# Performance work log

Hardware: AMD Instinct MI355X
Metric: run time of the kernel (lower is better)

The kernel has to match this reference:

```python
import jax, jax.numpy as jnp
import numpy as np
import math

S = 72; IMG_W = 640; IMG_H = 360; STRIDE = 16
IN_CH = 256; AFC = 64
FMAP_H = IMG_H // STRIDE  # 22
FMAP_W = IMG_W // STRIDE  # 40
N_OFFSETS = S
LEFT_ANGLES = [72., 60., 49., 39., 30., 22.]
RIGHT_ANGLES = [108., 120., 131., 141., 150., 158.]
BOTTOM_ANGLES = [165., 150., 141., 131., 120., 108., 100., 90., 80., 72., 60., 49., 39., 30., 15.]
BATCH = 8


def _gen_anchor(start, angle, cut):
    n = FMAP_H if cut else N_OFFSETS
    ys = np.linspace(1., 0., n)
    a = np.zeros(5 + n)
    sx, sy = start
    a[2] = 1. - sy
    a[3] = sx
    a[5:] = (sx + (1. - ys - 1. + sy) / math.tan(angle * math.pi / 180.)) * IMG_W
    return a


def _gen_side(angles, nb, x=None, y=None):
    if x is None:
        starts = [(xx, y) for xx in np.linspace(1., 0., nb)]
    else:
        starts = [(x, yy) for yy in np.linspace(1., 0., nb)]
    anc = np.stack([_gen_anchor(s, a, False) for s in starts for a in angles])
    cut = np.stack([_gen_anchor(s, a, True) for s in starts for a in angles])
    return anc, cut


def build_anchor_tables():
    la, lc = _gen_side(LEFT_ANGLES, 72, x=0.)
    ra, rc = _gen_side(RIGHT_ANGLES, 72, x=1.)
    ba, bc = _gen_side(BOTTOM_ANGLES, 128, y=1.)
    anchors = np.concatenate([la, ba, ra]).astype(np.float32)  # [P, 5+S]
    cuts = np.concatenate([lc, bc, rc])                        # [P, 5+fmap_h]
    xs = np.flip(np.round(cuts[:, 5:] / STRIDE), axis=1).astype(np.int64)
    cut_xs = np.clip(xs, 0, FMAP_W - 1).astype(np.int32)       # [P, fmap_h]
    invalid = (xs < 0) | (xs > FMAP_W)                         # faithful to original (> not >=)
    return anchors, cut_xs, invalid


def setup_inputs():
    key = jax.random.key(0)
    ks = jax.random.split(key, 6)
    anchors, cut_xs, invalid = build_anchor_tables()
    P = anchors.shape[0]  # 2784
    D = AFC * FMAP_H      # 1408
    s = 0.02
    return {
        "x": jax.random.normal(ks[0], (BATCH, IN_CH, FMAP_H, FMAP_W), jnp.float32),
        "conv_w": jax.random.normal(ks[1], (AFC, IN_CH), jnp.float32) * s,
        "conv_b": jnp.zeros((AFC,), jnp.float32),
        "att_w": jax.random.normal(ks[2], (P - 1, D), jnp.float32) * s,
        "att_b": jnp.zeros((P - 1,), jnp.float32),
        "cls_w": jax.random.normal(ks[3], (2, 2 * D), jnp.float32) * s,
        "cls_b": jnp.zeros((2,), jnp.float32),
        "so_w": jax.random.normal(ks[4], (1, 2 * D), jnp.float32) * s,
        "so_b": jnp.zeros((1,), jnp.float32),
        "reg_w": jax.random.normal(ks[5], (N_OFFSETS + 1, 2 * D), jnp.float32) * s,
        "reg_b": jnp.zeros((N_OFFSETS + 1,), jnp.float32),
        "anchors": jnp.asarray(anchors),
        "cut_xs": jnp.asarray(cut_xs),
        "invalid_mask": jnp.asarray(invalid),
    }


def reference(x, conv_w, conv_b, att_w, att_b, cls_w, cls_b, so_w, so_b, reg_w, reg_b, anchors, cut_xs, invalid_mask):
    B = x.shape[0]
    P, H = cut_xs.shape
    # 1x1 conv
    feat = jnp.einsum('bchw,oc->bohw', x, conv_w) + conv_b[None, :, None, None]
    # fused anchor feature gather: rois[b,p,c,h] = feat[b,c,h,cut_xs[p,h]]
    rois = feat[:, :, jnp.arange(H)[None, :], cut_xs]           # [B,C,P,H]
    rois = jnp.transpose(rois, (0, 2, 1, 3))                    # [B,P,C,H]
    rois = jnp.where(invalid_mask[None, :, None, :], 0., rois)
    D = rois.shape[2] * H
    baf = rois.reshape(B, P, D)
    scores = baf.reshape(B * P, D) @ att_w.T + att_b
    attention = jax.nn.softmax(scores, axis=1).reshape(B, P, P - 1)
    # off-diagonal scatter (replaces torch eye/nonzero trick): M[b,i,j]=attention[b,i,j'] for j!=i, diag 0
    i_idx = jnp.arange(P)[:, None]
    j_off = jnp.arange(P - 1)[None, :]
    tgt_j = jnp.where(j_off < i_idx, j_off, j_off + 1)          # [P,P-1]
    M = jnp.zeros((B, P, P), x.dtype).at[:, jnp.broadcast_to(i_idx, (P, P - 1)), tgt_j].set(attention)
    # (baf^T @ M^T)^T == M @ baf
    att_feats = jnp.einsum('bpq,bqd->bpd', M, baf)
    feats = jnp.concatenate([att_feats, baf], axis=2).reshape(B * P, 2 * D)
    cls = (feats @ cls_w.T + cls_b).reshape(B, P, 2)
    so = jax.nn.sigmoid(feats @ so_w.T + so_b).reshape(B, P, 1)
    reg = (feats @ reg_w.T + reg_b).reshape(B, P, N_OFFSETS + 1)
    anc = jnp.broadcast_to(anchors[None], (B, P, anchors.shape[1]))
    reg_proposals = jnp.concatenate([cls, (anc[:, :, 2:3] + so) * 0.5, anc[:, :, 3:4], anc[:, :, 4:] + reg], axis=2)
    return reg_proposals, M, feat
```

## Files before the change

### kernel.cpp

```cpp
#include <hip/hip_runtime.h>
#include <stdint.h>

#define PTOT 2784
#define PM1  2783
#define DDIM 1408
#define NB   8
#define ROWS 22272
#define KHEAD 2816
#define MROW 2816
#define BTROWS 1536

typedef __attribute__((ext_vector_type(8))) short bf16x8;
typedef __attribute__((ext_vector_type(4))) float f32x4;
typedef long i64f8;

__device__ __forceinline__ short f2bf_rne(float x) {
    uint32_t u = __float_as_uint(x);
    u += 0x7fffu + ((u >> 16) & 1u);
    return (short)(u >> 16);
}
__device__ __forceinline__ float bf2f(short s) {
    return __uint_as_float((uint32_t)(unsigned short)s << 16);
}

__device__ __forceinline__ unsigned char f2e4m3(float x) {
    uint32_t u = __float_as_uint(x);
    uint32_t sgn = (u >> 24) & 0x80u;
    uint32_t ax = u & 0x7fffffffu;
    ax += 0x7ffffu + ((ax >> 20) & 1u);
    if (ax >= 0x43E80000u) return (unsigned char)(sgn | 0x7Eu);
    if (ax < 0x3C800000u) return (unsigned char)sgn;
    uint32_t e = (ax >> 23) - 120u;
    uint32_t m = (ax >> 20) & 7u;
    return (unsigned char)(sgn | (e << 3) | m);
}

__device__ __forceinline__ void gld16(const void* g, void* l) {
    __builtin_amdgcn_global_load_lds(
        (const __attribute__((address_space(1))) void*)(uintptr_t)g,
        (__attribute__((address_space(3))) void*)(uint32_t)(uintptr_t)l,
        16, 0, 0);
}

#define VMW(N) asm volatile("s_waitcnt vmcnt(" #N ")" ::: "memory")

__global__ __launch_bounds__(256) void k_conv(
    const float* __restrict__ x, const float* __restrict__ w,
    const float* __restrict__ cb, float* __restrict__ feat) {
  __shared__ float xs[256 * 32];
  int b = blockIdx.x / 28;
  int t0 = (blockIdx.x % 28) * 32;
  int t = threadIdx.x;
  for (int i = t; i < 256 * 32; i += 256) {
    int c = i >> 5, pos = i & 31;
    int hw = t0 + pos;
    xs[i] = (hw < 880) ? x[((size_t)b * 256 + c) * 880 + hw] : 0.f;
  }
  __syncthreads();
  int o = t & 63, g = t >> 6;
  float acc[8];
#pragma unroll
  for (int pp = 0; pp < 8; ++pp) acc[pp] = cb[o];
  const float* wr = w + o * 256;
  for (int c = 0; c < 256; ++c) {
    float wv = wr[c];
#pragma unroll
    for (int pp = 0; pp < 8; ++pp) acc[pp] += wv * xs[c * 32 + g + pp * 4];
  }
#pragma unroll
  for (int pp = 0; pp < 8; ++pp) {
    int hw = t0 + g + pp * 4;
    if (hw < 880) feat[((size_t)b * 64 + o) * 880 + hw] = acc[pp];
  }
}

__global__ __launch_bounds__(256) void k_prep(
    const float* __restrict__ att_w, const float* __restrict__ cls_w,
    const float* __restrict__ so_w, const float* __restrict__ reg_w,
    const float* __restrict__ cls_b, const float* __restrict__ so_b,
    const float* __restrict__ reg_b,
    short* __restrict__ attw, short* __restrict__ wbf,
    float* __restrict__ bias80, float* __restrict__ M,
    unsigned char* __restrict__ Mbf8, unsigned char* __restrict__ bafT8,
    short* __restrict__ Msc) {
  const int64_t n_attw = (int64_t)2816 * DDIM;
  const int64_t n_w = 80 * (int64_t)KHEAD;
  const int64_t n_pa = (int64_t)NB * MROW * 32;
  const int64_t n_pb = (int64_t)NB * BTROWS * 32;
  const int64_t total = n_attw + n_w + 80 + ROWS + n_pa + n_pb;
  for (int64_t i = (int64_t)blockIdx.x * 256 + threadIdx.x; i < total;
       i += (int64_t)gridDim.x * 256) {
    if (i < n_attw) {
      int j = (int)(i / DDIM), k = (int)(i - (int64_t)j * DDIM);
      float v = (j < PM1) ? att_w[(size_t)j * DDIM + k] : 0.f;
      attw[i] = f2bf_rne(v);
    } else if (i < n_attw + n_w) {
      int64_t ii = i - n_attw;
      int n = (int)(ii / KHEAD), k = (int)(ii - (int64_t)n * KHEAD);
      float v = 0.f;
      if (n < 2) v = cls_w[n * KHEAD + k];
      else if (n == 2) v = so_w[k];
      else if (n < 76) v = reg_w[(size_t)(n - 3) * KHEAD + k];
      wbf[ii] = f2bf_rne(v);
    } else if (i < n_attw + n_w + 80) {
      int n = (int)(i - n_attw - n_w);
      float v = 0.f;
      if (n < 2) v = cls_b[n];
      else if (n == 2) v = so_b[0];
      else if (n < 76) v = reg_b[n - 3];
      bias80[n] = v;
    } else if (i < n_attw + n_w + 80 + ROWS) {
      int r = (int)(i - n_attw - n_w - 80);
      int p = r % PTOT;
      M[(size_t)r * PTOT + p] = -1e30f;
      if (Msc) Msc[(size_t)r * PTOT + p] = f2bf_rne(-1e30f);
    } else if (i < n_attw + n_w + 80 + ROWS + n_pa) {
      int64_t ii = i - n_attw - n_w - 80 - ROWS;
      int64_t row = ii >> 5; int c = (int)(ii & 31);
      Mbf8[row * 2816 + 2784 + c] = 0;
    } else {
      int64_t ii = i - n_attw - n_w - 80 - ROWS - n_pa;
      int64_t row = ii >> 5; int c = (int)(ii & 31);
      bafT8[row * 2816 + 2784 + c] = 0;
    }
  }
}

__global__ __launch_bounds__(256) void k_gather(
    const float* __restrict__ feat, const int* __restrict__ cutx,
    const unsigned char* __restrict__ inval,
    short* __restrict__ baf, unsigned char* __restrict__ bafT8) {
  int p0 = blockIdx.x * 64, d0 = blockIdx.y * 64, b = blockIdx.z;
  __shared__ short tile[64][72];
  int t = threadIdx.x;
  for (int i = t; i < 64 * 64; i += 256) {
    int pl = i >> 6, dl = i & 63;
    int p = p0 + pl, d = d0 + dl;
    float v = 0.f;
    if (p < PTOT && d < DDIM) {
      int c = d / 22, h = d - c * 22;
      if (!inval[p * 22 + h]) {
        int xc = cutx[p * 22 + h];
        v = feat[(((size_t)b * 64 + c) * 22 + h) * 40 + xc];
      }
    }
    tile[pl][dl] = f2bf_rne(v);
  }
  __syncthreads();
  if (d0 < DDIM) {
    for (int u = t; u < 512; u += 256) {
      int pl = u >> 3, dg = u & 7;
      int p = p0 + pl;
      if (p < PTOT) {
        bf16x8 v;
#pragma unroll
        for (int e = 0; e < 8; ++e) v[e] = tile[pl][dg * 8 + e];
        *(bf16x8*)&baf[((size_t)b * PTOT + p) * DDIM + d0 + dg * 8] = v;
      }
    }
  }
  for (int u = t; u < 512; u += 256) {
    int dl = u >> 3, pg = u & 7;
    int pbase = p0 + pg * 8;
    if (pbase + 7 < PTOT) {
      unsigned long long pk = 0;
#pragma unroll
      for (int e = 0; e < 8; ++e) {
        float fv = bf2f(tile[pg * 8 + e][dl]);
        pk |= (unsigned long long)f2e4m3(fv) << (8 * e);
      }
      *(unsigned long long*)&bafT8[((size_t)b * BTROWS + d0 + dl) * 2816 + pbase] = pk;
    }
  }
}

#define SC_TILE(OFF_, S_, SN_, STAGE_, VM_)                                    \
  {                                                                            \
    const char* cb_ = sm + (S_) * 16384;                                       \
    if (STAGE_) {                                                              \
      char* nb_ = sm + (SN_) * 16384;                                          \
      gld16(gA0 + (OFF_), nb_ + dd0);                                          \
      gld16(gA1 + (OFF_), nb_ + dd1);                                          \
      gld16(gB0 + (OFF_), nb_ + 8192 + dd0);                                   \
      gld16(gB1 + (OFF_), nb_ + 8192 + dd1);                                   \
    }                                                                          \
    if ((VM_) == 8) VMW(8); else if ((VM_) == 4) VMW(4); else VMW(0);          \
    __builtin_amdgcn_s_barrier();                                              \
    bf16x8 av[4], bv[4];                                                       \
    _Pragma("unroll") for (int i = 0; i < 4; ++i)                              \
      av[i] = *(const bf16x8*)(cb_ + offA[i]);                                 \
    _Pragma("unroll") for (int i = 0; i < 4; ++i)                              \
      bv[i] = *(const bf16x8*)(cb_ + 8192 + offB[i]);                          \
    _Pragma("unroll") for (int mi = 0; mi < 4; ++mi)                           \
      _Pragma("unroll") for (int ni = 0; ni < 4; ++ni)                         \
        acc[mi][ni] = __builtin_amdgcn_mfma_f32_16x16x32_bf16(                 \
            av[mi], bv[ni], acc[mi][ni], 0, 0, 0);                             \
    __builtin_amdgcn_s_barrier();                                              \
  }

template<int OUTMODE>
__global__ __launch_bounds__(256) void k_scores(
    const short* __restrict__ baf, const short* __restrict__ attw,
    const float* __restrict__ att_b, float* __restrict__ Mout,
    short* __restrict__ Msc) {
  __shared__ char sm[49152];
  int wg = blockIdx.x;
  int xcd = wg & 7, lin = wg >> 3;
  int wgid = (xcd < 4) ? xcd * 479 + lin : 1916 + (xcd - 4) * 478 + lin;
  int it = wgid / 22, nt = wgid - it * 22;
  int m0 = it * 128, n0 = nt * 128;

  int t = threadIdx.x, w = t >> 6, l = t & 63;
  int lr = l & 15, lg = l >> 4;
  int wr = w >> 1, wc = w & 1;

  const char* gA0; const char* gA1; const char* gB0; const char* gB1;
  int dd0, dd1;
  {
    int o0 = w * 2048 + l * 16;
    int o1 = o0 + 1024;
    int r0_ = o0 >> 6, c0 = (o0 & 63) ^ (((o0 >> 7) & 3) << 4);
    int r1_ = o1 >> 6, c1 = (o1 & 63) ^ (((o1 >> 7) & 3) << 4);
    gA0 = (const char*)(baf + (size_t)(m0 + r0_) * DDIM) + c0;
    gA1 = (const char*)(baf + (size_t)(m0 + r1_) * DDIM) + c1;
    gB0 = (const char*)(attw + (size_t)(n0 + r0_) * DDIM) + c0;
    gB1 = (const char*)(attw + (size_t)(n0 + r1_) * DDIM) + c1;
    dd0 = o0; dd1 = o1;
  }
  int offA[4], offB[4];
#pragma unroll
  for (int i = 0; i < 4; ++i) {
    int xa = (wr * 64 + i * 16 + lr) * 64 + lg * 16;
    offA[i] = xa ^ (((xa >> 7) & 3) << 4);
    int xb = (wc * 64 + i * 16 + lr) * 64 + lg * 16;
    offB[i] = xb ^ (((xb >> 7) & 3) << 4);
  }

  f32x4 acc[4][4];
  const f32x4 fz = {0.f, 0.f, 0.f, 0.f};
#pragma unroll
  for (int mi = 0; mi < 4; ++mi)
#pragma unroll
    for (int ni = 0; ni < 4; ++ni) acc[mi][ni] = fz;

  gld16(gA0, sm + dd0);            gld16(gA1, sm + dd1);
  gld16(gB0, sm + 8192 + dd0);     gld16(gB1, sm + 8192 + dd1);
  gld16(gA0 + 64, sm + 16384 + dd0);        gld16(gA1 + 64, sm + 16384 + dd1);
  gld16(gB0 + 64, sm + 16384 + 8192 + dd0); gld16(gB1 + 64, sm + 16384 + 8192 + dd1);

  for (int q = 0; q < 14; ++q) {
    SC_TILE(128, 0, 2, 1, 8);
    SC_TILE(192, 1, 0, 1, 8);
    SC_TILE(256, 2, 1, 1, 8);
    gA0 += 192; gA1 += 192; gB0 += 192; gB1 += 192;
  }
  SC_TILE(0, 0, 0, 0, 4);
  SC_TILE(0, 1, 0, 0, 0);

#pragma unroll
  for (int mi = 0; mi < 4; ++mi) {
#pragma unroll
    for (int rg = 0; rg < 4; ++rg) {
      int gmi = m0 + wr * 64 + mi * 16 + lg * 4 + rg;
      int i = gmi % PTOT;
#pragma unroll
      for (int ni = 0; ni < 4; ++ni) {
        int j = n0 + wc * 64 + ni * 16 + lr;
        if (j < PM1) {
          int q2 = j + (j >= i);
          float v = acc[mi][ni][rg] + att_b[j];
          if (OUTMODE == 0) Mout[(size_t)gmi * PTOT + q2] = v;
          else              Msc[(size_t)gmi * PTOT + q2] = f2bf_rne(v);
        }
      }
    }
  }
}

#define AF_TILE(OFF_, S_, SN_, STAGE_, VM_)                                    \
  {                                                                            \
    const char* cb_ = sm + (S_) * 16384;                                       \
    if (STAGE_) {                                                              \
      char* nb_ = sm + (SN_) * 16384;                                          \
      gld16(gA0 + (OFF_), nb_ + dd0);                                          \
      gld16(gA1 + (OFF_), nb_ + dd1);                                          \
      gld16(gB0 + (OFF_), nb_ + 8192 + dd0);                                   \
      gld16(gB1 + (OFF_), nb_ + 8192 + dd1);                                   \
    }                                                                          \
    if ((VM_) == 8) VMW(8); else if ((VM_) == 4) VMW(4); else VMW(0);          \
    __builtin_amdgcn_s_barrier();                                              \
    _Pragma("unroll") for (int ks = 0; ks < 2; ++ks) {                         \
      i64f8 av[4], bv[4];                                                      \
      _Pragma("unroll") for (int i = 0; i < 4; ++i)                            \
        av[i] = *(const i64f8*)(cb_ + offA[i * 2 + ks]);                       \
      _Pragma("unroll") for (int i = 0; i < 4; ++i)                            \
        bv[i] = *(const i64f8*)(cb_ + 8192 + offB[i * 2 + ks]);                \
      _Pragma("unroll") for (int mi = 0; mi < 4; ++mi)                         \
        _Pragma("unroll") for (int ni = 0; ni < 4; ++ni)                       \
          acc[mi][ni] = __builtin_amdgcn_mfma_f32_16x16x32_fp8_fp8(            \
              av[mi], bv[ni], acc[mi][ni], 0, 0, 0);                           \
    }                                                                          \
    __builtin_amdgcn_s_barrier();                                              \
  }

__global__ __launch_bounds__(256) void k_attfeat8(
    const unsigned char* __restrict__ Mbf8,
    const unsigned char* __restrict__ bafT8,
    short* __restrict__ attf) {
  __shared__ char sm[49152];
  int wg = blockIdx.x;
  int wgid = (wg & 7) * 242 + (wg >> 3);
  int bb = wgid / 242;
  int rem = wgid - bb * 242;
  int it = rem / 11, nt = rem - it * 11;
  int m0 = it * 128, n0 = nt * 128;
  const unsigned char* Ab = Mbf8 + ((size_t)bb * MROW + m0) * 2816;
  const unsigned char* Bb = bafT8 + ((size_t)bb * BTROWS + n0) * 2816;

  int t = threadIdx.x, w = t >> 6, l = t & 63;
  int lr = l & 15, lg = l >> 4;
  int wr = w >> 1, wc = w & 1;

  const char* gA0; const char* gA1; const char* gB0; const char* gB1;
  int dd0, dd1;
  {
    int o0 = t * 16;
    int o1 = o0 + 4096;
    int r0_ = o0 >> 6, c0 = (o0 & 63) ^ (((o0 >> 7) & 3) << 4);
    int r1_ = o1 >> 6, c1 = (o1 & 63) ^ (((o1 >> 7) & 3) << 4);
    gA0 = (const char*)Ab + (size_t)r0_ * 2816 + c0;
    gA1 = (const char*)Ab + (size_t)r1_ * 2816 + c1;
    gB0 = (const char*)Bb + (size_t)r0_ * 2816 + c0;
    gB1 = (const char*)Bb + (size_t)r1_ * 2816 + c1;
    dd0 = o0; dd1 = o1;
  }
  int offA[8], offB[8];
#pragma unroll
  for (int i = 0; i < 4; ++i) {
#pragma unroll
    for (int ks = 0; ks < 2; ++ks) {
      int xa = (wr * 64 + i * 16 + lr) * 64 + ks * 32 + lg * 8;
      offA[i * 2 + ks] = xa ^ (((xa >> 7) & 3) << 4);
      int xb = (wc * 64 + i * 16 + lr) * 64 + ks * 32 + lg * 8;
      offB[i * 2 + ks] = xb ^ (((xb >> 7) & 3) << 4);
    }
  }

  f32x4 acc[4][4];
  const f32x4 fz = {0.f, 0.f, 0.f, 0.f};
#pragma unroll
  for (int mi = 0; mi < 4; ++mi)
#pragma unroll
    for (int ni = 0; ni < 4; ++ni) acc[mi][ni] = fz;

  gld16(gA0, sm + dd0);            gld16(gA1, sm + dd1);
  gld16(gB0, sm + 8192 + dd0);     gld16(gB1, sm + 8192 + dd1);
  gld16(gA0 + 64, sm + 16384 + dd0);        gld16(gA1 + 64, sm + 16384 + dd1);
  gld16(gB0 + 64, sm + 16384 + 8192 + dd0); gld16(gB1 + 64, sm + 16384 + 8192 + dd1);

  for (int q = 0; q < 14; ++q) {
    AF_TILE(128, 0, 2, 1, 8);
    AF_TILE(192, 1, 0, 1, 8);
    AF_TILE(256, 2, 1, 1, 8);
    gA0 += 192; gA1 += 192; gB0 += 192; gB1 += 192;
  }
  AF_TILE(0, 0, 0, 0, 4);
  AF_TILE(0, 1, 0, 0, 0);

  const float US = 1.0f / 1024.0f;
#pragma unroll
  for (int mi = 0; mi < 4; ++mi) {
#pragma unroll
    for (int rg = 0; rg < 4; ++rg) {
      int i = m0 + wr * 64 + mi * 16 + lg * 4 + rg;
      if (i < PTOT) {
        short* arow = attf + ((size_t)(bb * PTOT + i)) * DDIM + n0 + wc * 64;
#pragma unroll
        for (int ni = 0; ni < 4; ++ni)
          arow[ni * 16 + lr] = f2bf_rne(acc[mi][ni][rg] * US);
      }
    }
  }
}

template<int INMODE>
__global__ __launch_bounds__(256) void k_softmax(float* __restrict__ M,
                                                 unsigned char* __restrict__ Mbf8,
                                                 const short* __restrict__ Msc) {
  __shared__ float red[8];
  int r = blockIdx.x;
  int b = r / PTOT, p = r - b * PTOT;
  float* pr = M + (size_t)r * PTOT;
  const short* ms = INMODE ? (Msc + (size_t)r * PTOT) : (const short*)nullptr;
  unsigned char* mb = Mbf8 + ((size_t)b * MROW + p) * 2816;
  int t = threadIdx.x;
  bool has2 = (t < 348 - 256);
  float v0[8], v1[8];
  float mx = -3.0e38f;
  if (INMODE == 0) {
    f32x4 a0 = *(const f32x4*)(pr + t * 8);
    f32x4 a1 = *(const f32x4*)(pr + t * 8 + 4);
#pragma unroll
    for (int e = 0; e < 4; ++e) { v0[e] = a0[e]; v0[4 + e] = a1[e]; }
  } else {
    bf16x8 a = *(const bf16x8*)(ms + t * 8);
#pragma unroll
    for (int e = 0; e < 8; ++e) v0[e] = bf2f(a[e]);
  }
#pragma unroll
  for (int e = 0; e < 8; ++e) mx = fmaxf(mx, v0[e]);
  if (has2) {
    if (INMODE == 0) {
      f32x4 b0 = *(const f32x4*)(pr + (256 + t) * 8);
      f32x4 b1 = *(const f32x4*)(pr + (256 + t) * 8 + 4);
#pragma unroll
      for (int e = 0; e < 4; ++e) { v1[e] = b0[e]; v1[4 + e] = b1[e]; }
    } else {
      bf16x8 bb = *(const bf16x8*)(ms + (256 + t) * 8);
#pragma unroll
      for (int e = 0; e < 8; ++e) v1[e] = bf2f(bb[e]);
    }
#pragma unroll
    for (int e = 0; e < 8; ++e) mx = fmaxf(mx, v1[e]);
  }
#pragma unroll
  for (int off = 32; off; off >>= 1) mx = fmaxf(mx, __shfl_xor(mx, off));
  if ((t & 63) == 0) red[t >> 6] = mx;
  __syncthreads();
  mx = fmaxf(fmaxf(red[0], red[1]), fmaxf(red[2], red[3]));
  float s = 0.f;
#pragma unroll
  for (int e = 0; e < 8; ++e) { v0[e] = __expf(v0[e] - mx); s += v0[e]; }
  if (has2) {
#pragma unroll
    for (int e = 0; e < 8; ++e) { v1[e] = __expf(v1[e] - mx); s += v1[e]; }
  }
#pragma unroll
  for (int off = 32; off; off >>= 1) s += __shfl_xor(s, off);
  if ((t & 63) == 0) red[4 + (t >> 6)] = s;
  __syncthreads();
  s = (red[4] + red[5]) + (red[6] + red[7]);
  float inv = 1.f / s;
  float invs = inv * 1024.f;
  {
    f32x4 o0, o1; unsigned long long pk = 0;
#pragma unroll
    for (int e = 0; e < 8; ++e) {
      float wv = v0[e] * inv;
      if (e < 4) o0[e] = wv; else o1[e - 4] = wv;
      pk |= (unsigned long long)f2e4m3(v0[e] * invs) << (8 * e);
    }
    *(f32x4*)(pr + t * 8) = o0;
    *(f32x4*)(pr + t * 8 + 4) = o1;
    *(unsigned long long*)(mb + t * 8) = pk;
  }
  if (has2) {
    f32x4 o0, o1; unsigned long long pk = 0;
#pragma unroll
    for (int e = 0; e < 8; ++e) {
      float wv = v1[e] * inv;
      if (e < 4) o0[e] = wv; else o1[e - 4] = wv;
      pk |= (unsigned long long)f2e4m3(v1[e] * invs) << (8 * e);
    }
    *(f32x4*)(pr + (256 + t) * 8) = o0;
    *(f32x4*)(pr + (256 + t) * 8 + 4) = o1;
    *(unsigned long long*)(mb + (256 + t) * 8) = pk;
  }
}

__global__ __launch_bounds__(256) void k_head(
    const short* __restrict__ attf, const short* __restrict__ baf,
    const short* __restrict__ wbf, const float* __restrict__ bias80,
    const float* __restrict__ anch, float* __restrict__ out) {
  __shared__ short smA[64 * 32];
  __shared__ short smB[80 * 32];
  int r0 = blockIdx.x * 64;
  int t = threadIdx.x, wid = t >> 6, lane = t & 63;
  int rowa = t >> 2, kg = t & 3;
  const short* sA_att = attf + (size_t)(r0 + rowa) * DDIM + kg * 8;
  const short* sA_baf = baf + (size_t)(r0 + rowa) * DDIM + kg * 8;
  const short* sB0 = wbf + (size_t)rowa * KHEAD + kg * 8;
  const short* sB1 = wbf + (size_t)(64 + (t >> 2)) * KHEAD + (t & 3) * 8;
  char* lA = (char*)smA + wid * 1024;
  char* lB0 = (char*)smB + wid * 1024;
  char* lB1 = (char*)smB + 4096;
  int lr = lane & 15, lg = lane >> 4;
  const short* pA = smA + (wid * 16 + lr) * 32 + lg * 8;
  const short* pB = smB + lr * 32 + lg * 8;
  f32x4 acc[5];
  const f32x4 fz = {0.f, 0.f, 0.f, 0.f};
  for (int i2 = 0; i2 < 5; ++i2) acc[i2] = fz;
  for (int ks = 0; ks < 88; ++ks) {
    const short* sA = (ks < 44) ? (sA_att + ks * 32) : (sA_baf + (ks - 44) * 32);
    gld16(sA, lA);
    gld16(sB0 + ks * 32, lB0);
    if (t < 64) gld16(sB1 + ks * 32, lB1);
    __syncthreads();
    bf16x8 a = *(const bf16x8*)pA;
#pragma unroll
    for (int ni = 0; ni < 5; ++ni) {
      bf16x8 b = *(const bf16x8*)(pB + ni * 512);
      acc[ni] = __builtin_amdgcn_mfma_f32_16x16x32_bf16(a, b, acc[ni], 0, 0, 0);
    }
    __syncthreads();
  }
#pragma unroll
  for (int ni = 0; ni < 5; ++ni) {
#pragma unroll
    for (int rg = 0; rg < 4; ++rg) {
      int n = ni * 16 + lr;
      int i = wid * 16 + lg * 4 + rg;
      int rgl = r0 + i;
      int p = rgl % PTOT;
      float v = acc[ni][rg] + bias80[n];
      if (n < 2) {
        out[(size_t)rgl * 77 + n] = v;
      } else if (n == 2) {
        out[(size_t)rgl * 77 + 2] =
            (anch[(size_t)p * 77 + 2] + 1.f / (1.f + __expf(-v))) * 0.5f;
        out[(size_t)rgl * 77 + 3] = anch[(size_t)p * 77 + 3];
      } else if (n < 76) {
        out[(size_t)rgl * 77 + n + 1] = v + anch[(size_t)p * 77 + n + 1];
      }
    }
  }
}

extern "C" void kernel_launch(void* const* d_in, const int* in_sizes, int n_in,
                              void* d_out, int out_size, void* d_ws, size_t ws_size,
                              hipStream_t stream) {
  const float* x      = (const float*)d_in[0];
  const float* conv_w = (const float*)d_in[1];
  const float* conv_b = (const float*)d_in[2];
  const float* att_w  = (const float*)d_in[3];
  const float* att_b  = (const float*)d_in[4];
  const float* cls_w  = (const float*)d_in[5];
  const float* cls_b  = (const float*)d_in[6];
  const float* so_w   = (const float*)d_in[7];
  const float* so_b   = (const float*)d_in[8];
  const float* reg_w  = (const float*)d_in[9];
  const float* reg_b  = (const float*)d_in[10];
  const float* anchors= (const float*)d_in[11];
  const int*   cut_xs = (const int*)d_in[12];
  const unsigned char* invalid = (const unsigned char*)d_in[13];

  float* out_rp = (float*)d_out;
  float* Mmat = out_rp + (size_t)ROWS * 77;
  float* feat = Mmat + (size_t)ROWS * PTOT;

  char* wsp = (char*)d_ws;
  short* baf            = (short*)wsp;
  unsigned char* bafT8  = (unsigned char*)(wsp + 62717952ULL);
  unsigned char* Mbf8   = (unsigned char*)(wsp + 97320960ULL);
  short* attw           = (short*)(wsp + 160759808ULL);
  short* wbf            = (short*)(wsp + 168689664ULL);
  float* bias80         = (float*)(wsp + 169140224ULL);
  short* attf           = (short*)(wsp + 169140736ULL);
  short* Msc            = (short*)(wsp + 231858688ULL);
  const size_t WS_FAST  = 231858688ULL + 124010496ULL;

  bool fast = (ws_size >= WS_FAST);

  k_conv<<<224, 256, 0, stream>>>(x, conv_w, conv_b, feat);
  k_prep<<<2048, 256, 0, stream>>>(att_w, cls_w, so_w, reg_w, cls_b, so_b, reg_b,
                                   attw, wbf, bias80, Mmat, Mbf8, bafT8,
                                   fast ? Msc : (short*)nullptr);
  k_gather<<<dim3(44, 24, 8), 256, 0, stream>>>(feat, cut_xs, invalid, baf, bafT8);
  if (fast) {
    k_scores<1><<<3828, 256, 0, stream>>>(baf, attw, att_b, (float*)nullptr, Msc);
    k_softmax<1><<<ROWS, 256, 0, stream>>>(Mmat, Mbf8, Msc);
  } else {
    k_scores<0><<<3828, 256, 0, stream>>>(baf, attw, att_b, Mmat, (short*)nullptr);
    k_softmax<0><<<ROWS, 256, 0, stream>>>(Mmat, Mbf8, (const short*)nullptr);
  }
  k_attfeat8<<<1936, 256, 0, stream>>>(Mbf8, bafT8, attf);
  k_head<<<348, 256, 0, stream>>>(attf, baf, wbf, bias80, anchors, out_rp);
}
```

Before: 685.4 us.

## Widen score and attention-feature GEMM tiles to 128x256 with 8-wave blocks

Both the attention-score GEMM and the fp8 attention-feature GEMM move from 128x128 tiles on 256-thread blocks to 128x256 tiles on 512-thread blocks with a 4x2 wave layout. Each thread now issues three 16-byte global-to-LDS loads per stage instead of four, and the vmcnt waits drop to match. The grids and XCD remapping are rewritten for the new tile counts, and a column guard is added where the feature dimension is padded. The aim is to reuse each A tile across twice as many output columns and so cut global and LDS traffic per MFMA. The cost is more LDS per block (72 KB in a triple-buffered ring), which lowers how many blocks fit per CU, and fewer blocks overall, which can hurt load balance.

After: 637.2 us. 7.0% less time.

```diff
diff --git a/kernel.cpp b/kernel.cpp
--- a/kernel.cpp
+++ b/kernel.cpp
@@ -176,15 +176,14 @@
 
 #define SC_TILE(OFF_, S_, SN_, STAGE_, VM_)                                    \
   {                                                                            \
-    const char* cb_ = sm + (S_) * 16384;                                       \
+    const char* cb_ = sm + (S_) * 24576;                                       \
     if (STAGE_) {                                                              \
-      char* nb_ = sm + (SN_) * 16384;                                          \
-      gld16(gA0 + (OFF_), nb_ + dd0);                                          \
-      gld16(gA1 + (OFF_), nb_ + dd1);                                          \
-      gld16(gB0 + (OFF_), nb_ + 8192 + dd0);                                   \
-      gld16(gB1 + (OFF_), nb_ + 8192 + dd1);                                   \
+      char* nb_ = sm + (SN_) * 24576;                                          \
+      gld16(gA0 + (OFF_), nb_ + ddA);                                          \
+      gld16(gB0 + (OFF_), nb_ + 8192 + ddA);                                   \
+      gld16(gB1 + (OFF_), nb_ + 16384 + ddA);                                  \
     }                                                                          \
-    if ((VM_) == 8) VMW(8); else if ((VM_) == 4) VMW(4); else VMW(0);          \
+    if ((VM_) == 6) VMW(6); else if ((VM_) == 3) VMW(3); else VMW(0);          \
     __builtin_amdgcn_s_barrier();                                              \
     bf16x8 av[4], bv[4];                                                       \
     _Pragma("unroll") for (int i = 0; i < 4; ++i)                              \
@@ -199,33 +198,33 @@
   }
 
 template<int OUTMODE>
-__global__ __launch_bounds__(256) void k_scores(
+__global__ __launch_bounds__(512, 4) void k_scores(
     const short* __restrict__ baf, const short* __restrict__ attw,
     const float* __restrict__ att_b, float* __restrict__ Mout,
     short* __restrict__ Msc) {
-  __shared__ char sm[49152];
+  __shared__ char sm[73728];
   int wg = blockIdx.x;
   int xcd = wg & 7, lin = wg >> 3;
-  int wgid = (xcd < 4) ? xcd * 479 + lin : 1916 + (xcd - 4) * 478 + lin;
-  int it = wgid / 22, nt = wgid - it * 22;
-  int m0 = it * 128, n0 = nt * 128;
+  int wgid = (xcd < 2) ? xcd * 240 + lin : 480 + (xcd - 2) * 239 + lin;
+  int it = wgid / 11, nt = wgid - it * 11;
+  int m0 = it * 128, n0 = nt * 256;
 
   int t = threadIdx.x, w = t >> 6, l = t & 63;
   int lr = l & 15, lg = l >> 4;
-  int wr = w >> 1, wc = w & 1;
-
-  const char* gA0; const char* gA1; const char* gB0; const char* gB1;
-  int dd0, dd1;
+  int wr = w >> 2, wc = w & 3;
+
+  const char* gA0; const char* gB0; const char* gB1;
+  int ddA = t * 16;
   {
-    int o0 = w * 2048 + l * 16;
-    int o1 = o0 + 1024;
-    int r0_ = o0 >> 6, c0 = (o0 & 63) ^ (((o0 >> 7) & 3) << 4);
-    int r1_ = o1 >> 6, c1 = (o1 & 63) ^ (((o1 >> 7) & 3) << 4);
-    gA0 = (const char*)(baf + (size_t)(m0 + r0_) * DDIM) + c0;
-    gA1 = (const char*)(baf + (size_t)(m0 + r1_) * DDIM) + c1;
-    gB0 = (const char*)(attw + (size_t)(n0 + r0_) * DDIM) + c0;
-    gB1 = (const char*)(attw + (size_t)(n0 + r1_) * DDIM) + c1;
-    dd0 = o0; dd1 = o1;
+    int oA = t * 16;
+    int rA = oA >> 6, cA = (oA & 63) ^ (((oA >> 7) & 3) << 4);
+    gA0 = (const char*)(baf + (size_t)(m0 + rA) * DDIM) + cA;
+    int oB0 = t * 16;
+    int rB0 = oB0 >> 6, cB0 = (oB0 & 63) ^ (((oB0 >> 7) & 3) << 4);
+    gB0 = (const char*)(attw + (size_t)(n0 + rB0) * DDIM) + cB0;
+    int oB1 = 8192 + t * 16;
+    int rB1 = oB1 >> 6, cB1 = (oB1 & 63) ^ (((oB1 >> 7) & 3) << 4);
+    gB1 = (const char*)(attw + (size_t)(n0 + rB1) * DDIM) + cB1;
   }
   int offA[4], offB[4];
 #pragma unroll
@@ -243,18 +242,20 @@
 #pragma unroll
     for (int ni = 0; ni < 4; ++ni) acc[mi][ni] = fz;
 
-  gld16(gA0, sm + dd0);            gld16(gA1, sm + dd1);
-  gld16(gB0, sm + 8192 + dd0);     gld16(gB1, sm + 8192 + dd1);
-  gld16(gA0 + 64, sm + 16384 + dd0);        gld16(gA1 + 64, sm + 16384 + dd1);
-  gld16(gB0 + 64, sm + 16384 + 8192 + dd0); gld16(gB1 + 64, sm + 16384 + 8192 + dd1);
+  gld16(gA0, sm + ddA);
+  gld16(gB0, sm + 8192 + ddA);
+  gld16(gB1, sm + 16384 + ddA);
+  gld16(gA0 + 64, sm + 24576 + ddA);
+  gld16(gB0 + 64, sm + 24576 + 8192 + ddA);
+  gld16(gB1 + 64, sm + 24576 + 16384 + ddA);
 
   for (int q = 0; q < 14; ++q) {
-    SC_TILE(128, 0, 2, 1, 8);
-    SC_TILE(192, 1, 0, 1, 8);
-    SC_TILE(256, 2, 1, 1, 8);
-    gA0 += 192; gA1 += 192; gB0 += 192; gB1 += 192;
-  }
-  SC_TILE(0, 0, 0, 0, 4);
+    SC_TILE(128, 0, 2, 1, 6);
+    SC_TILE(192, 1, 0, 1, 6);
+    SC_TILE(256, 2, 1, 1, 6);
+    gA0 += 192; gB0 += 192; gB1 += 192;
+  }
+  SC_TILE(0, 0, 0, 0, 3);
   SC_TILE(0, 1, 0, 0, 0);
 
 #pragma unroll
@@ -279,15 +280,14 @@
 
 #define AF_TILE(OFF_, S_, SN_, STAGE_, VM_)                                    \
   {                                                                            \
-    const char* cb_ = sm + (S_) * 16384;                                       \
+    const char* cb_ = sm + (S_) * 24576;                                       \
     if (STAGE_) {                                                              \
-      char* nb_ = sm + (SN_) * 16384;                                          \
-      gld16(gA0 + (OFF_), nb_ + dd0);                                          \
-      gld16(gA1 + (OFF_), nb_ + dd1);                                          \
-      gld16(gB0 + (OFF_), nb_ + 8192 + dd0);                                   \
-      gld16(gB1 + (OFF_), nb_ + 8192 + dd1);                                   \
+      char* nb_ = sm + (SN_) * 24576;                                          \
+      gld16(gA0 + (OFF_), nb_ + ddA);                                          \
+      gld16(gB0 + (OFF_), nb_ + 8192 + ddA);                                   \
+      gld16(gB1 + (OFF_), nb_ + 16384 + ddA);                                  \
     }                                                                          \
-    if ((VM_) == 8) VMW(8); else if ((VM_) == 4) VMW(4); else VMW(0);          \
+    if ((VM_) == 6) VMW(6); else if ((VM_) == 3) VMW(3); else VMW(0);          \
     __builtin_amdgcn_s_barrier();                                              \
     _Pragma("unroll") for (int ks = 0; ks < 2; ++ks) {                         \
       i64f8 av[4], bv[4];                                                      \
@@ -303,36 +303,36 @@
     __builtin_amdgcn_s_barrier();                                              \
   }
 
-__global__ __launch_bounds__(256) void k_attfeat8(
+__global__ __launch_bounds__(512, 4) void k_attfeat8(
     const unsigned char* __restrict__ Mbf8,
     const unsigned char* __restrict__ bafT8,
     short* __restrict__ attf) {
-  __shared__ char sm[49152];
+  __shared__ char sm[73728];
   int wg = blockIdx.x;
-  int wgid = (wg & 7) * 242 + (wg >> 3);
-  int bb = wgid / 242;
-  int rem = wgid - bb * 242;
-  int it = rem / 11, nt = rem - it * 11;
-  int m0 = it * 128, n0 = nt * 128;
+  int wgid = (wg & 7) * 132 + (wg >> 3);
+  int bb = wgid / 132;
+  int rem = wgid - bb * 132;
+  int it = rem / 6, dt = rem - it * 6;
+  int m0 = it * 128, n0 = dt * 256;
   const unsigned char* Ab = Mbf8 + ((size_t)bb * MROW + m0) * 2816;
   const unsigned char* Bb = bafT8 + ((size_t)bb * BTROWS + n0) * 2816;
 
   int t = threadIdx.x, w = t >> 6, l = t & 63;
   int lr = l & 15, lg = l >> 4;
-  int wr = w >> 1, wc = w & 1;
-
-  const char* gA0; const char* gA1; const char* gB0; const char* gB1;
-  int dd0, dd1;
+  int wr = w >> 2, wc = w & 3;
+
+  const char* gA0; const char* gB0; const char* gB1;
+  int ddA = t * 16;
   {
-    int o0 = t * 16;
-    int o1 = o0 + 4096;
-    int r0_ = o0 >> 6, c0 = (o0 & 63) ^ (((o0 >> 7) & 3) << 4);
-    int r1_ = o1 >> 6, c1 = (o1 & 63) ^ (((o1 >> 7) & 3) << 4);
-    gA0 = (const char*)Ab + (size_t)r0_ * 2816 + c0;
-    gA1 = (const char*)Ab + (size_t)r1_ * 2816 + c1;
-    gB0 = (const char*)Bb + (size_t)r0_ * 2816 + c0;
-    gB1 = (const char*)Bb + (size_t)r1_ * 2816 + c1;
-    dd0 = o0; dd1 = o1;
+    int oA = t * 16;
+    int rA = oA >> 6, cA = (oA & 63) ^ (((oA >> 7) & 3) << 4);
+    gA0 = (const char*)Ab + (size_t)rA * 2816 + cA;
+    int oB0 = t * 16;
+    int rB0 = oB0 >> 6, cB0 = (oB0 & 63) ^ (((oB0 >> 7) & 3) << 4);
+    gB0 = (const char*)Bb + (size_t)rB0 * 2816 + cB0;
+    int oB1 = 8192 + t * 16;
+    int rB1 = oB1 >> 6, cB1 = (oB1 & 63) ^ (((oB1 >> 7) & 3) << 4);
+    gB1 = (const char*)Bb + (size_t)rB1 * 2816 + cB1;
   }
   int offA[8], offB[8];
 #pragma unroll
@@ -353,18 +353,20 @@
 #pragma unroll
     for (int ni = 0; ni < 4; ++ni) acc[mi][ni] = fz;
 
-  gld16(gA0, sm + dd0);            gld16(gA1, sm + dd1);
-  gld16(gB0, sm + 8192 + dd0);     gld16(gB1, sm + 8192 + dd1);
-  gld16(gA0 + 64, sm + 16384 + dd0);        gld16(gA1 + 64, sm + 16384 + dd1);
-  gld16(gB0 + 64, sm + 16384 + 8192 + dd0); gld16(gB1 + 64, sm + 16384 + 8192 + dd1);
+  gld16(gA0, sm + ddA);
+  gld16(gB0, sm + 8192 + ddA);
+  gld16(gB1, sm + 16384 + ddA);
+  gld16(gA0 + 64, sm + 24576 + ddA);
+  gld16(gB0 + 64, sm + 24576 + 8192 + ddA);
+  gld16(gB1 + 64, sm + 24576 + 16384 + ddA);
 
   for (int q = 0; q < 14; ++q) {
-    AF_TILE(128, 0, 2, 1, 8);
-    AF_TILE(192, 1, 0, 1, 8);
-    AF_TILE(256, 2, 1, 1, 8);
-    gA0 += 192; gA1 += 192; gB0 += 192; gB1 += 192;
-  }
-  AF_TILE(0, 0, 0, 0, 4);
+    AF_TILE(128, 0, 2, 1, 6);
+    AF_TILE(192, 1, 0, 1, 6);
+    AF_TILE(256, 2, 1, 1, 6);
+    gA0 += 192; gB0 += 192; gB1 += 192;
+  }
+  AF_TILE(0, 0, 0, 0, 3);
   AF_TILE(0, 1, 0, 0, 0);
 
   const float US = 1.0f / 1024.0f;
@@ -374,10 +376,12 @@
     for (int rg = 0; rg < 4; ++rg) {
       int i = m0 + wr * 64 + mi * 16 + lg * 4 + rg;
       if (i < PTOT) {
-        short* arow = attf + ((size_t)(bb * PTOT + i)) * DDIM + n0 + wc * 64;
-#pragma unroll
-        for (int ni = 0; ni < 4; ++ni)
-          arow[ni * 16 + lr] = f2bf_rne(acc[mi][ni][rg] * US);
+        short* arow = attf + ((size_t)(bb * PTOT + i)) * DDIM;
+#pragma unroll
+        for (int ni = 0; ni < 4; ++ni) {
+          int d = n0 + wc * 64 + ni * 16 + lr;
+          if (d < DDIM) arow[d] = f2bf_rne(acc[mi][ni][rg] * US);
+        }
       }
     }
   }
@@ -567,12 +571,12 @@
                                    fast ? Msc : (short*)nullptr);
   k_gather<<<dim3(44, 24, 8), 256, 0, stream>>>(feat, cut_xs, invalid, baf, bafT8);
   if (fast) {
-    k_scores<1><<<3828, 256, 0, stream>>>(baf, attw, att_b, (float*)nullptr, Msc);
+    k_scores<1><<<1914, 512, 0, stream>>>(baf, attw, att_b, (float*)nullptr, Msc);
     k_softmax<1><<<ROWS, 256, 0, stream>>>(Mmat, Mbf8, Msc);
   } else {
-    k_scores<0><<<3828, 256, 0, stream>>>(baf, attw, att_b, Mmat, (short*)nullptr);
+    k_scores<0><<<1914, 512, 0, stream>>>(baf, attw, att_b, Mmat, (short*)nullptr);
     k_softmax<0><<<ROWS, 256, 0, stream>>>(Mmat, Mbf8, (const short*)nullptr);
   }
-  k_attfeat8<<<1936, 256, 0, stream>>>(Mbf8, bafT8, attf);
+  k_attfeat8<<<1056, 512, 0, stream>>>(Mbf8, bafT8, attf);
   k_head<<<348, 256, 0, stream>>>(attf, baf, wbf, bias80, anchors, out_rp);
 }
```
